# Kernel tuning notes

Hardware: AMD Instinct MI355X
Metric: run time of the kernel (lower is better)

The kernel has to match this reference:

```python
import jax, jax.numpy as jnp
import numpy as np

S = 2048        # seqlen_sum (packed tokens)
DIM = 4096
N_HEADS = 32
N_KV_HEADS = 8
HEAD_DIM = 128
ROPE_THETA = 10000.0


def setup_inputs() -> dict:
    key = jax.random.key(0)
    ks = jax.random.split(key, 5)
    x = jax.random.normal(ks[0], (S, DIM), dtype=jnp.float32)
    # true RoPE frequencies: freqs_cis = exp(i * pos * theta^{-2j/d})
    inv_freq = ROPE_THETA ** (-jnp.arange(0, HEAD_DIM, 2, dtype=jnp.float32) / HEAD_DIM)  # [64]
    angles = jnp.arange(S, dtype=jnp.float32)[:, None] * inv_freq[None, :]               # [S,64]
    freqs_cos = jnp.cos(angles)
    freqs_sin = jnp.sin(angles)
    scale = 0.02
    wq = jax.random.normal(ks[1], (DIM, N_HEADS * HEAD_DIM), dtype=jnp.float32) * scale
    wk = jax.random.normal(ks[2], (DIM, N_KV_HEADS * HEAD_DIM), dtype=jnp.float32) * scale
    wv = jax.random.normal(ks[3], (DIM, N_KV_HEADS * HEAD_DIM), dtype=jnp.float32) * scale
    wo = jax.random.normal(ks[4], (N_HEADS * HEAD_DIM, DIM), dtype=jnp.float32) * scale
    return {"x": x, "freqs_cos": freqs_cos, "freqs_sin": freqs_sin,
            "wq": wq, "wk": wk, "wv": wv, "wo": wo}


def _apply_rope(t, cos, sin):
    # t: [S, H, D]; pairs (t0,t1) along last dim form complex numbers (torch view_as_complex)
    tr = t.reshape(t.shape[0], t.shape[1], -1, 2)
    t0, t1 = tr[..., 0], tr[..., 1]
    c = cos[:, None, :]  # [S,1,D/2]
    s = sin[:, None, :]
    o0 = t0 * c - t1 * s
    o1 = t0 * s + t1 * c
    return jnp.stack([o0, o1], axis=-1).reshape(t.shape)


def reference(x, freqs_cos, freqs_sin, wq, wk, wv, wo):
    repeats = N_HEADS // N_KV_HEADS
    xq = (x @ wq).reshape(S, N_HEADS, HEAD_DIM)
    xk = (x @ wk).reshape(S, N_KV_HEADS, HEAD_DIM)
    xv = (x @ wv).reshape(S, N_KV_HEADS, HEAD_DIM)
    xq = _apply_rope(xq, freqs_cos, freqs_sin)
    xk = _apply_rope(xk, freqs_cos, freqs_sin)
    # GQA: repeat_interleave KV heads (cache=None path -> key/val = xk/xv)
    key = jnp.repeat(xk, repeats, axis=1)  # [S, N_HEADS, D]
    val = jnp.repeat(xv, repeats, axis=1)
    scale = HEAD_DIM ** -0.5
    scores = jnp.einsum('qhd,khd->hqk', xq, key) * scale   # [H,S,S]
    attn = jax.nn.softmax(scores, axis=-1)
    out = jnp.einsum('hqk,khd->qhd', attn, val)            # [S,H,D]
    return out.reshape(S, N_HEADS * HEAD_DIM) @ wo
```

## Files before the change

### kernel.cpp

```cpp
#include <hip/hip_runtime.h>

#define S_LEN 2048
#define DIM   4096
#define NH    32
#define NKV   8
#define HD    128
#define QKV_LD 6144
#define KOFF 4096
#define VOFF 5120

typedef __attribute__((ext_vector_type(8))) __bf16 bf16x8;
typedef __attribute__((ext_vector_type(4))) float  floatx4;

union U8 { unsigned short u[8]; bf16x8 v; int4 i4; };
union U32x4 { unsigned int u[4]; bf16x8 v; };

__device__ inline unsigned short f2bf(float f) {
  unsigned int u = __float_as_uint(f);
  u += 0x7fff + ((u >> 16) & 1);
  return (unsigned short)(u >> 16);
}
__device__ inline float bf2f(unsigned short h) {
  return __uint_as_float(((unsigned int)h) << 16);
}

__device__ inline floatx4 mfma16(bf16x8 a, bf16x8 b, floatx4 c) {
  return __builtin_amdgcn_mfma_f32_16x16x32_bf16(a, b, c, 0, 0, 0);
}

typedef __attribute__((address_space(1))) void GV;
typedef __attribute__((address_space(3))) void LV;
__device__ inline void gload_lds16(const unsigned short* g, unsigned short* l) {
  __builtin_amdgcn_global_load_lds((GV*)g, (LV*)l, 16, 0, 0);
}

__global__ __launch_bounds__(256) void transpose_cvt(
    const float* __restrict__ in, unsigned short* __restrict__ outT, int K, int N)
{
  __shared__ float t[32][33];
  const int n0 = blockIdx.x * 32, k0 = blockIdx.y * 32;
  const int tx = threadIdx.x & 31, ty = threadIdx.x >> 5;
#pragma unroll
  for (int i = 0; i < 32; i += 8)
    t[ty + i][tx] = in[(size_t)(k0 + ty + i) * N + n0 + tx];
  __syncthreads();
#pragma unroll
  for (int i = 0; i < 32; i += 8)
    outT[(size_t)(n0 + ty + i) * K + k0 + tx] = f2bf(t[tx][ty + i]);
}

__global__ __launch_bounds__(256) void cvt_f32_bf16(
    const float* __restrict__ in, unsigned short* __restrict__ out)
{
  int i = (blockIdx.x * 256 + threadIdx.x) * 8;
  float4 a = *(const float4*)(in + i);
  float4 b = *(const float4*)(in + i + 4);
  U8 t;
  t.u[0] = f2bf(a.x); t.u[1] = f2bf(a.y); t.u[2] = f2bf(a.z); t.u[3] = f2bf(a.w);
  t.u[4] = f2bf(b.x); t.u[5] = f2bf(b.y); t.u[6] = f2bf(b.z); t.u[7] = f2bf(b.w);
  *(int4*)(out + i) = t.i4;
}

template<bool C_F32>
__global__ __launch_bounds__(256) void gemm_bt(
    const unsigned short* __restrict__ A,
    const unsigned short* __restrict__ Bt,
    void* __restrict__ C_, int M, int N, int K)
{
  __shared__ __align__(16) unsigned short As[128 * 32];
  __shared__ __align__(16) unsigned short Bs[128 * 32];

  const int tid  = threadIdx.x;
  const int wave = tid >> 6;
  const int lane = tid & 63;
  const int quad = lane >> 4;
  const int l16  = lane & 15;
  const int m0 = blockIdx.y * 128, n0 = blockIdx.x * 128;
  const int mw = (wave & 1) * 64, nw = (wave >> 1) * 64;

  floatx4 acc[4][4] = {};

  for (int k0 = 0; k0 < K; k0 += 32) {
#pragma unroll
    for (int p = 0; p < 2; p++) {
      int c = wave * 128 + p * 64 + lane;
      gload_lds16(A  + (size_t)(m0 + (c >> 2)) * K + k0 + (c & 3) * 8,
                  As + (wave * 128 + p * 64) * 8);
      gload_lds16(Bt + (size_t)(n0 + (c >> 2)) * K + k0 + (c & 3) * 8,
                  Bs + (wave * 128 + p * 64) * 8);
    }
    __syncthreads();

    bf16x8 af[4], bf[4];
#pragma unroll
    for (int mt = 0; mt < 4; mt++)
      af[mt] = *(const bf16x8*)(As + (mw + mt * 16 + l16) * 32 + quad * 8);
#pragma unroll
    for (int nt = 0; nt < 4; nt++)
      bf[nt] = *(const bf16x8*)(Bs + (nw + nt * 16 + l16) * 32 + quad * 8);
#pragma unroll
    for (int mt = 0; mt < 4; mt++)
#pragma unroll
      for (int nt = 0; nt < 4; nt++)
        acc[mt][nt] = mfma16(af[mt], bf[nt], acc[mt][nt]);
    __syncthreads();
  }

#pragma unroll
  for (int mt = 0; mt < 4; mt++)
#pragma unroll
    for (int nt = 0; nt < 4; nt++)
#pragma unroll
      for (int i = 0; i < 4; i++) {
        int r = m0 + mw + mt * 16 + quad * 4 + i;
        int c = n0 + nw + nt * 16 + l16;
        if (C_F32) ((float*)C_)[(size_t)r * N + c] = acc[mt][nt][i];
        else ((unsigned short*)C_)[(size_t)r * N + c] = f2bf(acc[mt][nt][i]);
      }
}

__global__ __launch_bounds__(256) void rope_kernel(
    unsigned short* __restrict__ qkv,
    const float* __restrict__ fcos, const float* __restrict__ fsin)
{
  int idx = blockIdx.x * 256 + threadIdx.x;
  int p = idx & 63;
  int t = idx >> 6;
  int h = t % (NH + NKV);
  int s = t / (NH + NKV);

  float c  = fcos[s * 64 + p];
  float sn = fsin[s * 64 + p];
  const float qs = 0.08838834764831845f;

  unsigned short* base;
  float m;
  if (h < NH) { base = qkv + (size_t)s * QKV_LD + h * HD + p * 2; m = qs; }
  else { base = qkv + (size_t)s * QKV_LD + KOFF + (h - NH) * HD + p * 2; m = 1.f; }

  unsigned int both = *(const unsigned int*)base;
  float t0 = bf2f((unsigned short)(both & 0xffff));
  float t1 = bf2f((unsigned short)(both >> 16));
  unsigned int o0 = f2bf((t0 * c - t1 * sn) * m);
  unsigned int o1 = f2bf((t0 * sn + t1 * c) * m);
  *(unsigned int*)base = o0 | (o1 << 16);
}

__global__ __launch_bounds__(256) void vtrans_kernel(
    const unsigned short* __restrict__ qkv, unsigned short* __restrict__ vt)
{
  __shared__ unsigned short t[32][34];
  const int s0 = blockIdx.x * 32;
  const int d0 = blockIdx.y * 32;
  const int tx = threadIdx.x & 31, ty = threadIdx.x >> 5;
#pragma unroll
  for (int i = 0; i < 32; i += 8)
    t[ty + i][tx] = qkv[(size_t)(s0 + ty + i) * QKV_LD + VOFF + d0 + tx];
  __syncthreads();
#pragma unroll
  for (int i = 0; i < 32; i += 8)
    vt[(size_t)(d0 + ty + i) * S_LEN + s0 + tx] = t[tx][ty + i];
}

__global__ __launch_bounds__(256, 2) void attn_kernel(
    const unsigned short* __restrict__ qkv,
    const unsigned short* __restrict__ vt,
    unsigned short* __restrict__ o)
{
  __shared__ __align__(16) unsigned short Ks[2][64 * 136];
  __shared__ __align__(16) unsigned short Vs[2][128 * 72];

  const int h    = blockIdx.x;
  const int qblk = blockIdx.y;
  const int kvh  = h >> 2;
  const int tid  = threadIdx.x;
  const int lane = tid & 63;
  const int quad = lane >> 4;
  const int l16  = lane & 15;
  const int wave = tid >> 6;
  const int qr   = qblk * 128 + wave * 16;

  bf16x8 qf[2][4];
#pragma unroll
  for (int mt = 0; mt < 2; mt++)
#pragma unroll
    for (int ks = 0; ks < 4; ks++)
      qf[mt][ks] = *(const bf16x8*)(qkv + (size_t)(qr + mt * 64 + l16) * QKV_LD
                                    + h * HD + ks * 32 + quad * 8);

  floatx4 accO[2][8] = {};
  float l_i[2] = {0.f, 0.f};

  int4 pk[4], pv4[4];
#define LOAD_TILE(kb_) do {                                                     \
    _Pragma("unroll")                                                           \
    for (int j = 0; j < 4; j++) {                                               \
      int c = tid + 256 * j;                                                    \
      pk[j] = *(const int4*)(qkv + (size_t)((kb_) * 64 + (c >> 4)) * QKV_LD     \
                              + KOFF + kvh * HD + (c & 15) * 8);                \
      pv4[j] = *(const int4*)(vt + (size_t)(kvh * HD + (c >> 3)) * S_LEN        \
                              + (kb_) * 64 + (c & 7) * 8);                      \
    } } while (0)
#define STORE_TILE(b_) do {                                                     \
    _Pragma("unroll")                                                           \
    for (int j = 0; j < 4; j++) {                                               \
      int c = tid + 256 * j;                                                    \
      *(int4*)(Ks[b_] + (c >> 4) * 136 + (c & 15) * 8) = pk[j];                 \
      *(int4*)(Vs[b_] + (c >> 3) * 72 + (c & 7) * 8) = pv4[j];                  \
    } } while (0)

  LOAD_TILE(0);
  STORE_TILE(0);
  __syncthreads();

  const int srcA = ((quad & 1) << 5) | l16;
  const bool hi  = (quad & 2);

  for (int kb = 0; kb < S_LEN / 64; kb++) {
    const int cur = kb & 1;
    if (kb + 1 < S_LEN / 64) LOAD_TILE(kb + 1);

    const unsigned short* Ksc = Ks[cur];
    const unsigned short* Vsc = Vs[cur];

    floatx4 sacc[2][4] = {};
    __builtin_amdgcn_s_setprio(1);
#pragma unroll
    for (int ks = 0; ks < 4; ks++)
#pragma unroll
      for (int nt = 0; nt < 4; nt++) {
        bf16x8 kf = *(const bf16x8*)(Ksc + (nt * 16 + l16) * 136 + ks * 32 + quad * 8);
        sacc[0][nt] = mfma16(kf, qf[0][ks], sacc[0][nt]);
        sacc[1][nt] = mfma16(kf, qf[1][ks], sacc[1][nt]);
      }
    __builtin_amdgcn_s_setprio(0);

    unsigned int wp[2][2][4];
#pragma unroll
    for (int mt = 0; mt < 2; mt++) {
      float ls = 0.f;
#pragma unroll
      for (int nt = 0; nt < 4; nt++) {
        float e0 = __expf(sacc[mt][nt][0]);
        float e1 = __expf(sacc[mt][nt][1]);
        float e2 = __expf(sacc[mt][nt][2]);
        float e3 = __expf(sacc[mt][nt][3]);
        ls += (e0 + e1) + (e2 + e3);
        wp[mt][0][nt] = (unsigned int)f2bf(e0) | ((unsigned int)f2bf(e1) << 16);
        wp[mt][1][nt] = (unsigned int)f2bf(e2) | ((unsigned int)f2bf(e3) << 16);
      }
      l_i[mt] += ls;
    }

#pragma unroll
    for (int k2 = 0; k2 < 2; k2++) {
      bf16x8 paf[2];
#pragma unroll
      for (int mt = 0; mt < 2; mt++) {
        const int ntl = k2 * 2, nth = k2 * 2 + 1;
        unsigned int a0 = __shfl((int)wp[mt][0][ntl], srcA, 64);
        unsigned int b0 = __shfl((int)wp[mt][0][nth], srcA, 64);
        unsigned int a1 = __shfl((int)wp[mt][1][ntl], srcA, 64);
        unsigned int b1 = __shfl((int)wp[mt][1][nth], srcA, 64);
        unsigned int a2 = __shfl((int)wp[mt][0][ntl], srcA + 16, 64);
        unsigned int b2 = __shfl((int)wp[mt][0][nth], srcA + 16, 64);
        unsigned int a3 = __shfl((int)wp[mt][1][ntl], srcA + 16, 64);
        unsigned int b3 = __shfl((int)wp[mt][1][nth], srcA + 16, 64);
        U32x4 pw;
        pw.u[0] = hi ? b0 : a0;
        pw.u[1] = hi ? b1 : a1;
        pw.u[2] = hi ? b2 : a2;
        pw.u[3] = hi ? b3 : a3;
        paf[mt] = pw.v;
      }
      __builtin_amdgcn_s_setprio(1);
#pragma unroll
      for (int dt = 0; dt < 8; dt++) {
        bf16x8 vf = *(const bf16x8*)(Vsc + (dt * 16 + l16) * 72 + k2 * 32 + quad * 8);
        accO[0][dt] = mfma16(paf[0], vf, accO[0][dt]);
        accO[1][dt] = mfma16(paf[1], vf, accO[1][dt]);
      }
      __builtin_amdgcn_s_setprio(0);
    }

    if (kb + 1 < S_LEN / 64) STORE_TILE(cur ^ 1);
    __syncthreads();
  }

#pragma unroll
  for (int mt = 0; mt < 2; mt++) {
    l_i[mt] += __shfl_xor(l_i[mt], 16, 64);
    l_i[mt] += __shfl_xor(l_i[mt], 32, 64);
  }

#pragma unroll
  for (int mt = 0; mt < 2; mt++) {
    float lq[4];
#pragma unroll
    for (int i = 0; i < 4; i++) lq[i] = __shfl(l_i[mt], quad * 4 + i, 64);
#pragma unroll
    for (int dt = 0; dt < 8; dt++)
#pragma unroll
      for (int i = 0; i < 4; i++) {
        float val = accO[mt][dt][i] / lq[i];
        o[(size_t)(qr + mt * 64 + quad * 4 + i) * (NH * HD) + h * HD + dt * 16 + l16]
            = f2bf(val);
      }
  }
#undef LOAD_TILE
#undef STORE_TILE
}

extern "C" void kernel_launch(void* const* d_in, const int* in_sizes, int n_in,
                              void* d_out, int out_size, void* d_ws, size_t ws_size,
                              hipStream_t stream)
{
  const float* x    = (const float*)d_in[0];
  const float* fcos = (const float*)d_in[1];
  const float* fsin = (const float*)d_in[2];
  const float* wq   = (const float*)d_in[3];
  const float* wk   = (const float*)d_in[4];
  const float* wv   = (const float*)d_in[5];
  const float* wo   = (const float*)d_in[6];
  float* out = (float*)d_out;

  unsigned short* ws = (unsigned short*)d_ws;
  unsigned short* xb   = ws;
  unsigned short* wT   = xb   + (size_t)S_LEN * DIM;
  unsigned short* woT  = wT   + (size_t)QKV_LD * DIM;
  unsigned short* qkv  = woT  + (size_t)DIM * (NH * HD);
  unsigned short* vt   = qkv  + (size_t)S_LEN * QKV_LD;
  unsigned short* attn = vt   + (size_t)S_LEN * (NKV * HD);

  cvt_f32_bf16<<<(S_LEN * DIM) / (256 * 8), 256, 0, stream>>>(x, xb);
  transpose_cvt<<<dim3(DIM / 32, DIM / 32),        256, 0, stream>>>(wq, wT, DIM, DIM);
  transpose_cvt<<<dim3((NKV * HD) / 32, DIM / 32), 256, 0, stream>>>(wk, wT + (size_t)KOFF * DIM, DIM, NKV * HD);
  transpose_cvt<<<dim3((NKV * HD) / 32, DIM / 32), 256, 0, stream>>>(wv, wT + (size_t)VOFF * DIM, DIM, NKV * HD);
  transpose_cvt<<<dim3(DIM / 32, (NH * HD) / 32),  256, 0, stream>>>(wo, woT, NH * HD, DIM);

  gemm_bt<false><<<dim3(QKV_LD / 128, S_LEN / 128), 256, 0, stream>>>(xb, wT, qkv, S_LEN, QKV_LD, DIM);

  rope_kernel<<<(S_LEN * (NH + NKV) * 64) / 256, 256, 0, stream>>>(qkv, fcos, fsin);
  vtrans_kernel<<<dim3(S_LEN / 32, (NKV * HD) / 32), 256, 0, stream>>>(qkv, vt);

  attn_kernel<<<dim3(NH, S_LEN / 128), 256, 0, stream>>>(qkv, vt, attn);

  gemm_bt<true><<<dim3(DIM / 128, S_LEN / 128), 256, 0, stream>>>(attn, woT, out, S_LEN, DIM, NH * HD);
}
```

Baseline: 567.0 us.

## Replace GEMM kernel with 4-stage pipelined, swizzled, larger-tile 512-thread GEMM

Replaces the single-buffered 128x128 GEMM with a templated kernel that prefetches three K-slabs ahead into a 4-deep LDS ring using direct global-to-LDS loads. It waits with explicit vmcnt counters and s_barrier instead of two __syncthreads per slab. It also XOR-swizzles LDS chunks to reduce bank conflicts, remaps workgroups for L2 locality, raises MFMA priority, and uses 256x256 or 128x256 tiles with 8 waves. The aim is to hide global load latency and raise MFMA utilisation in the QKV and output projections. The trade-offs are higher LDS and register use, and hand-written waitcnt logic whose correctness depends on the compiler's instruction ordering.

Measured after the change: 615.0 us. 8.5% more time.

```diff
diff --git a/kernel.cpp b/kernel.cpp
--- a/kernel.cpp
+++ b/kernel.cpp
@@ -34,6 +34,14 @@
   __builtin_amdgcn_global_load_lds((GV*)g, (LV*)l, 16, 0, 0);
 }
 
+template<int N> __device__ __forceinline__ void vmcnt_wait() {
+  if constexpr (N == 8)      asm volatile("s_waitcnt vmcnt(8)" ::: "memory");
+  else if constexpr (N == 6) asm volatile("s_waitcnt vmcnt(6)" ::: "memory");
+  else if constexpr (N == 4) asm volatile("s_waitcnt vmcnt(4)" ::: "memory");
+  else if constexpr (N == 3) asm volatile("s_waitcnt vmcnt(3)" ::: "memory");
+  else                       asm volatile("s_waitcnt vmcnt(0)" ::: "memory");
+}
+
 __global__ __launch_bounds__(256) void transpose_cvt(
     const float* __restrict__ in, unsigned short* __restrict__ outT, int K, int N)
 {
@@ -61,61 +69,101 @@
   *(int4*)(out + i) = t.i4;
 }
 
-template<bool C_F32>
-__global__ __launch_bounds__(256) void gemm_bt(
+template<int BM, int BN, int WM, int WN, bool C_F32>
+__global__ __launch_bounds__(512, 2) void gemm_pipe(
     const unsigned short* __restrict__ A,
     const unsigned short* __restrict__ Bt,
     void* __restrict__ C_, int M, int N, int K)
 {
-  __shared__ __align__(16) unsigned short As[128 * 32];
-  __shared__ __align__(16) unsigned short Bs[128 * 32];
+  constexpr int MFRAG = BM / WM / 16;
+  constexpr int NFRAG = BN / WN / 16;
+  constexpr int LA = BM / 128;
+  constexpr int LB = BN / 128;
+  constexpr int L  = LA + LB;
+
+  __shared__ __align__(16) unsigned short As[4][BM * 32];
+  __shared__ __align__(16) unsigned short Bs[4][BN * 32];
+
+  const int nwg  = gridDim.x * gridDim.y;
+  const int bid0 = blockIdx.y * gridDim.x + blockIdx.x;
+  const int wg   = (bid0 & 7) * (nwg >> 3) + (bid0 >> 3);
+  const int bx = wg % gridDim.x, by = wg / gridDim.x;
+  const int m0 = by * BM, n0 = bx * BN;
 
   const int tid  = threadIdx.x;
-  const int wave = tid >> 6;
-  const int lane = tid & 63;
-  const int quad = lane >> 4;
-  const int l16  = lane & 15;
-  const int m0 = blockIdx.y * 128, n0 = blockIdx.x * 128;
-  const int mw = (wave & 1) * 64, nw = (wave >> 1) * 64;
-
-  floatx4 acc[4][4] = {};
-
-  for (int k0 = 0; k0 < K; k0 += 32) {
-#pragma unroll
-    for (int p = 0; p < 2; p++) {
-      int c = wave * 128 + p * 64 + lane;
-      gload_lds16(A  + (size_t)(m0 + (c >> 2)) * K + k0 + (c & 3) * 8,
-                  As + (wave * 128 + p * 64) * 8);
-      gload_lds16(Bt + (size_t)(n0 + (c >> 2)) * K + k0 + (c & 3) * 8,
-                  Bs + (wave * 128 + p * 64) * 8);
+  const int wave = tid >> 6, lane = tid & 63;
+  const int quad = lane >> 4, l16 = lane & 15;
+  const int wm = wave / WN, wn = wave % WN;
+  const int nslab = K >> 5;
+
+#define STAGE(t_) do {                                                          \
+    int b_ = (t_) & 3; int k0_ = (t_) * 32;                                     \
+    _Pragma("unroll")                                                           \
+    for (int s = 0; s < LA; s++) {                                              \
+      int c = s * 512 + wave * 64 + lane;                                       \
+      int row = c >> 2, cir = (c & 3) ^ ((row >> 1) & 3);                       \
+      gload_lds16(A + (size_t)(m0 + row) * K + k0_ + cir * 8,                   \
+                  &As[b_][(s * 512 + wave * 64) * 8]);                          \
+    }                                                                           \
+    _Pragma("unroll")                                                           \
+    for (int s = 0; s < LB; s++) {                                              \
+      int c = s * 512 + wave * 64 + lane;                                       \
+      int row = c >> 2, cir = (c & 3) ^ ((row >> 1) & 3);                       \
+      gload_lds16(Bt + (size_t)(n0 + row) * K + k0_ + cir * 8,                  \
+                  &Bs[b_][(s * 512 + wave * 64) * 8]);                          \
+    } } while (0)
+
+  floatx4 acc[MFRAG][NFRAG] = {};
+
+  STAGE(0); STAGE(1); STAGE(2);
+  vmcnt_wait<2 * L>();
+  __builtin_amdgcn_s_barrier();
+  __builtin_amdgcn_sched_barrier(0);
+
+  for (int t = 0; t < nslab; t++) {
+    if (t + 3 < nslab) STAGE(t + 3);
+
+    const unsigned short* Ab = As[t & 3];
+    const unsigned short* Bb = Bs[t & 3];
+    bf16x8 af[MFRAG], bf[NFRAG];
+#pragma unroll
+    for (int m = 0; m < MFRAG; m++) {
+      int row = wm * (MFRAG * 16) + m * 16 + l16;
+      af[m] = *(const bf16x8*)(Ab + row * 32 + (quad ^ ((row >> 1) & 3)) * 8);
     }
-    __syncthreads();
-
-    bf16x8 af[4], bf[4];
-#pragma unroll
-    for (int mt = 0; mt < 4; mt++)
-      af[mt] = *(const bf16x8*)(As + (mw + mt * 16 + l16) * 32 + quad * 8);
-#pragma unroll
-    for (int nt = 0; nt < 4; nt++)
-      bf[nt] = *(const bf16x8*)(Bs + (nw + nt * 16 + l16) * 32 + quad * 8);
-#pragma unroll
-    for (int mt = 0; mt < 4; mt++)
-#pragma unroll
-      for (int nt = 0; nt < 4; nt++)
-        acc[mt][nt] = mfma16(af[mt], bf[nt], acc[mt][nt]);
-    __syncthreads();
+#pragma unroll
+    for (int n = 0; n < NFRAG; n++) {
+      int row = wn * (NFRAG * 16) + n * 16 + l16;
+      bf[n] = *(const bf16x8*)(Bb + row * 32 + (quad ^ ((row >> 1) & 3)) * 8);
+    }
+
+    __builtin_amdgcn_s_setprio(1);
+#pragma unroll
+    for (int m = 0; m < MFRAG; m++)
+#pragma unroll
+      for (int n = 0; n < NFRAG; n++)
+        acc[m][n] = mfma16(af[m], bf[n], acc[m][n]);
+    __builtin_amdgcn_s_setprio(0);
+
+    if (t + 3 < nslab)      vmcnt_wait<2 * L>();
+    else if (t + 2 < nslab) vmcnt_wait<L>();
+    else if (t + 1 < nslab) vmcnt_wait<0>();
+    asm volatile("s_waitcnt lgkmcnt(0)" ::: "memory");
+    __builtin_amdgcn_s_barrier();
+    __builtin_amdgcn_sched_barrier(0);
   }
-
-#pragma unroll
-  for (int mt = 0; mt < 4; mt++)
-#pragma unroll
-    for (int nt = 0; nt < 4; nt++)
+#undef STAGE
+
+#pragma unroll
+  for (int m = 0; m < MFRAG; m++)
+#pragma unroll
+    for (int n = 0; n < NFRAG; n++)
 #pragma unroll
       for (int i = 0; i < 4; i++) {
-        int r = m0 + mw + mt * 16 + quad * 4 + i;
-        int c = n0 + nw + nt * 16 + l16;
-        if (C_F32) ((float*)C_)[(size_t)r * N + c] = acc[mt][nt][i];
-        else ((unsigned short*)C_)[(size_t)r * N + c] = f2bf(acc[mt][nt][i]);
+        int r = m0 + wm * (MFRAG * 16) + m * 16 + quad * 4 + i;
+        int c = n0 + wn * (NFRAG * 16) + n * 16 + l16;
+        if (C_F32) ((float*)C_)[(size_t)r * N + c] = acc[m][n][i];
+        else ((unsigned short*)C_)[(size_t)r * N + c] = f2bf(acc[m][n][i]);
       }
 }
 
@@ -338,12 +386,14 @@
   transpose_cvt<<<dim3((NKV * HD) / 32, DIM / 32), 256, 0, stream>>>(wv, wT + (size_t)VOFF * DIM, DIM, NKV * HD);
   transpose_cvt<<<dim3(DIM / 32, (NH * HD) / 32),  256, 0, stream>>>(wo, woT, NH * HD, DIM);
 
-  gemm_bt<false><<<dim3(QKV_LD / 128, S_LEN / 128), 256, 0, stream>>>(xb, wT, qkv, S_LEN, QKV_LD, DIM);
+  gemm_pipe<256, 256, 2, 4, false>
+      <<<dim3(QKV_LD / 256, S_LEN / 256), 512, 0, stream>>>(xb, wT, qkv, S_LEN, QKV_LD, DIM);
 
   rope_kernel<<<(S_LEN * (NH + NKV) * 64) / 256, 256, 0, stream>>>(qkv, fcos, fsin);
   vtrans_kernel<<<dim3(S_LEN / 32, (NKV * HD) / 32), 256, 0, stream>>>(qkv, vt);
 
   attn_kernel<<<dim3(NH, S_LEN / 128), 256, 0, stream>>>(qkv, vt, attn);
 
-  gemm_bt<true><<<dim3(DIM / 128, S_LEN / 128), 256, 0, stream>>>(attn, woT, out, S_LEN, DIM, NH * HD);
-}
+  gemm_pipe<128, 256, 2, 4, true>
+      <<<dim3(DIM / 256, S_LEN / 128), 512, 0, stream>>>(attn, woT, out, S_LEN, DIM, NH * HD);
+}
```

## Replace QKV projection GEMM with 256x256 8-wave pipelined GEMM kernel

Applied to the files above, without the earlier changes.

Adds a new gemm8 kernel that uses 256x256 tiles with 512 threads, double-buffered LDS filled by direct global-to-LDS loads with XOR swizzling, and a hand-interleaved schedule of quarter-tile loads and MFMA groups. It uses explicit vmcnt waits, barriers and s_setprio, plus a workgroup remap for L2 locality. The QKV projection now launches this kernel instead of gemm_bt. The larger tiles and overlapped loads aim to raise MFMA utilisation, but the grid shrinks to 24x8=192 blocks and 128 KB of LDS per block may limit occupancy.

Measured after the change: 567.3 us. No clear change (+0.1%).

```diff
diff --git a/kernel.cpp b/kernel.cpp
--- a/kernel.cpp
+++ b/kernel.cpp
@@ -34,6 +34,14 @@
   __builtin_amdgcn_global_load_lds((GV*)g, (LV*)l, 16, 0, 0);
 }
 
+template<int N> __device__ __forceinline__ void vmcnt_wait() {
+  if constexpr (N == 8)      asm volatile("s_waitcnt vmcnt(8)" ::: "memory");
+  else if constexpr (N == 6) asm volatile("s_waitcnt vmcnt(6)" ::: "memory");
+  else if constexpr (N == 4) asm volatile("s_waitcnt vmcnt(4)" ::: "memory");
+  else if constexpr (N == 2) asm volatile("s_waitcnt vmcnt(2)" ::: "memory");
+  else                       asm volatile("s_waitcnt vmcnt(0)" ::: "memory");
+}
+
 __global__ __launch_bounds__(256) void transpose_cvt(
     const float* __restrict__ in, unsigned short* __restrict__ outT, int K, int N)
 {
@@ -117,6 +125,156 @@
         if (C_F32) ((float*)C_)[(size_t)r * N + c] = acc[mt][nt][i];
         else ((unsigned short*)C_)[(size_t)r * N + c] = f2bf(acc[mt][nt][i]);
       }
+}
+
+template<bool C_F32>
+__global__ __launch_bounds__(512, 2) void gemm8(
+    const unsigned short* __restrict__ A,
+    const unsigned short* __restrict__ Bt,
+    void* __restrict__ C_, int M, int N, int K)
+{
+  __shared__ __align__(16) unsigned short As[2][256 * 64];
+  __shared__ __align__(16) unsigned short Bs[2][256 * 64];
+
+  const int nwg  = gridDim.x * gridDim.y;
+  const int bid0 = blockIdx.y * gridDim.x + blockIdx.x;
+  const int wg   = (bid0 & 7) * (nwg >> 3) + (bid0 >> 3);
+  const int bx = wg % gridDim.x, by = wg / gridDim.x;
+  const int m0 = by * 256, n0 = bx * 256;
+
+  const int tid  = threadIdx.x;
+  const int wave = tid >> 6, lane = tid & 63;
+  const int quad = lane >> 4, l16 = lane & 15;
+  const int wm = wave >> 2, wn = wave & 3;
+
+  floatx4 acc[8][4] = {};
+  bf16x8 af[4][2];
+  bf16x8 bfr[2][2][2];
+
+#define STAGE_A8(buf_, mq_, kt_) do {                                           \
+    _Pragma("unroll")                                                           \
+    for (int s = 0; s < 2; s++) {                                               \
+      int row = s * 128 + (mq_) * 64 + (tid >> 3);                              \
+      gload_lds16(A + (size_t)(m0 + row) * K + (kt_) * 64                       \
+                    + (((tid & 7) ^ (row & 7)) * 8),                            \
+                  &As[buf_][(s * 128 + (mq_) * 64 + wave * 8) * 64]);           \
+    } } while (0)
+
+#define STAGE_B8(buf_, nq_, kt_) do {                                           \
+    _Pragma("unroll")                                                           \
+    for (int s = 0; s < 2; s++) {                                               \
+      int c = s * 512 + tid;                                                    \
+      int row = (c >> 8) * 64 + (nq_) * 32 + ((c >> 3) & 31);                   \
+      gload_lds16(Bt + (size_t)(n0 + row) * K + (kt_) * 64                      \
+                    + (((tid & 7) ^ (row & 7)) * 8),                            \
+                  &Bs[buf_][((s * 2 + (wave >> 2)) * 64 + (nq_) * 32            \
+                            + (wave & 3) * 8) * 64]);                           \
+    } } while (0)
+
+#define LOAD_AF8(buf_, mq_) do {                                                \
+    _Pragma("unroll")                                                           \
+    for (int m = 0; m < 4; m++)                                                 \
+    _Pragma("unroll")                                                           \
+      for (int ks = 0; ks < 2; ks++) {                                          \
+        int row = wm * 128 + (mq_) * 64 + m * 16 + l16;                         \
+        af[m][ks] = *(const bf16x8*)(&As[buf_][row * 64                         \
+                       + (((ks * 4 + quad) ^ (l16 & 7)) * 8)]);                 \
+      } } while (0)
+
+#define LOAD_BF8(buf_, nq_) do {                                                \
+    _Pragma("unroll")                                                           \
+    for (int n = 0; n < 2; n++)                                                 \
+    _Pragma("unroll")                                                           \
+      for (int ks = 0; ks < 2; ks++) {                                          \
+        int row = wn * 64 + (nq_) * 32 + n * 16 + l16;                          \
+        bfr[nq_][n][ks] = *(const bf16x8*)(&Bs[buf_][row * 64                   \
+                       + (((ks * 4 + quad) ^ (l16 & 7)) * 8)]);                 \
+      } } while (0)
+
+#define MFMA_Q8(mq_, nq_) do {                                                  \
+    __builtin_amdgcn_s_setprio(1);                                              \
+    _Pragma("unroll")                                                           \
+    for (int ks = 0; ks < 2; ks++)                                              \
+    _Pragma("unroll")                                                           \
+      for (int m = 0; m < 4; m++)                                               \
+      _Pragma("unroll")                                                         \
+        for (int n = 0; n < 2; n++)                                             \
+          acc[(mq_) * 4 + m][(nq_) * 2 + n] = mfma16(af[m][ks],                 \
+              bfr[nq_][n][ks], acc[(mq_) * 4 + m][(nq_) * 2 + n]);              \
+    __builtin_amdgcn_s_setprio(0);                                              \
+  } while (0)
+
+#define BAR_MID() do { __builtin_amdgcn_s_barrier();                            \
+    asm volatile("s_waitcnt lgkmcnt(0)" ::: "memory");                          \
+    __builtin_amdgcn_sched_barrier(0); } while (0)
+
+#define GATE(n_) do { vmcnt_wait<n_>();                                         \
+    __builtin_amdgcn_sched_barrier(0);                                          \
+    __builtin_amdgcn_s_barrier(); } while (0)
+
+#define ENDP() __builtin_amdgcn_s_barrier()
+
+  const int NIT = K >> 7;
+
+  STAGE_A8(0, 0, 0); STAGE_B8(0, 0, 0); STAGE_B8(0, 1, 0); STAGE_A8(0, 1, 0);
+  vmcnt_wait<4>();
+  __builtin_amdgcn_s_barrier();
+
+  for (int i = 0; i < NIT; i++) {
+    const int t1 = 2 * i + 1, t2 = 2 * i + 2;
+    const bool more = (i + 1 < NIT);
+    LOAD_AF8(0, 0); LOAD_BF8(0, 0);
+    STAGE_A8(1, 0, t1);
+    BAR_MID(); MFMA_Q8(0, 0); GATE(4);
+    LOAD_BF8(0, 1);
+    STAGE_B8(1, 0, t1);
+    BAR_MID(); MFMA_Q8(0, 1); GATE(4);
+    LOAD_AF8(0, 1);
+    STAGE_B8(1, 1, t1);
+    BAR_MID(); MFMA_Q8(1, 1); ENDP();
+    STAGE_A8(1, 1, t1);
+    BAR_MID(); MFMA_Q8(1, 0); GATE(4);
+    LOAD_AF8(1, 0); LOAD_BF8(1, 0);
+    if (more) STAGE_A8(0, 0, t2);
+    BAR_MID(); MFMA_Q8(0, 0);
+    if (more) GATE(4); else GATE(2);
+    LOAD_BF8(1, 1);
+    if (more) STAGE_B8(0, 0, t2);
+    BAR_MID(); MFMA_Q8(0, 1);
+    if (more) GATE(4); else GATE(0);
+    LOAD_AF8(1, 1);
+    if (more) STAGE_B8(0, 1, t2);
+    BAR_MID(); MFMA_Q8(1, 1); ENDP();
+    if (more) STAGE_A8(0, 1, t2);
+    BAR_MID(); MFMA_Q8(1, 0);
+    if (more) GATE(4); else ENDP();
+  }
+
+#undef STAGE_A8
+#undef STAGE_B8
+#undef LOAD_AF8
+#undef LOAD_BF8
+#undef MFMA_Q8
+#undef BAR_MID
+#undef GATE
+#undef ENDP
+
+#pragma unroll
+  for (int mq = 0; mq < 2; mq++)
+#pragma unroll
+    for (int m = 0; m < 4; m++)
+#pragma unroll
+      for (int nq = 0; nq < 2; nq++)
+#pragma unroll
+        for (int n = 0; n < 2; n++)
+#pragma unroll
+          for (int i2 = 0; i2 < 4; i2++) {
+            int r = m0 + wm * 128 + mq * 64 + m * 16 + quad * 4 + i2;
+            int c = n0 + wn * 64 + nq * 32 + n * 16 + l16;
+            float v = acc[mq * 4 + m][nq * 2 + n][i2];
+            if (C_F32) ((float*)C_)[(size_t)r * N + c] = v;
+            else ((unsigned short*)C_)[(size_t)r * N + c] = f2bf(v);
+          }
 }
 
 __global__ __launch_bounds__(256) void rope_kernel(
@@ -338,7 +496,8 @@
   transpose_cvt<<<dim3((NKV * HD) / 32, DIM / 32), 256, 0, stream>>>(wv, wT + (size_t)VOFF * DIM, DIM, NKV * HD);
   transpose_cvt<<<dim3(DIM / 32, (NH * HD) / 32),  256, 0, stream>>>(wo, woT, NH * HD, DIM);
 
-  gemm_bt<false><<<dim3(QKV_LD / 128, S_LEN / 128), 256, 0, stream>>>(xb, wT, qkv, S_LEN, QKV_LD, DIM);
+  gemm8<false>
+      <<<dim3(QKV_LD / 256, S_LEN / 256), 512, 0, stream>>>(xb, wT, qkv, S_LEN, QKV_LD, DIM);
 
   rope_kernel<<<(S_LEN * (NH + NKV) * 64) / 256, 256, 0, stream>>>(qkv, fcos, fsin);
   vtrans_kernel<<<dim3(S_LEN / 32, (NKV * HD) / 32), 256, 0, stream>>>(qkv, vt);
```
